# Optimization experiments

Measured on AMD Instinct MI355X. Metric: run time of the kernel, lower is better.

## Reference

```python
import jax, jax.numpy as jnp
import numpy as np

B, T, D, H = 64, 2048, 256, 256

def setup_inputs() -> dict:
    key = jax.random.key(0)
    k_x, k_z, k_r, k_h = jax.random.split(key, 4)
    gate_in = D + H
    # lecun_normal: std = 1/sqrt(fan_in)
    s = 1.0 / np.sqrt(gate_in)
    return {
        "x": jax.random.normal(k_x, (B, T, D), dtype=jnp.float32),
        "W_z": jax.random.normal(k_z, (gate_in, H), dtype=jnp.float32) * s,
        "b_z": jnp.zeros((H,), dtype=jnp.float32),
        "W_r": jax.random.normal(k_r, (gate_in, H), dtype=jnp.float32) * s,
        "b_r": jnp.zeros((H,), dtype=jnp.float32),
        "W_h": jax.random.normal(k_h, (gate_in, H), dtype=jnp.float32) * s,
        "b_h": jnp.zeros((H,), dtype=jnp.float32),
    }

def reference(x, W_z, b_z, W_r, b_r, W_h, b_h):
    Bx, Tx, Dx = x.shape
    Hx = W_z.shape[1]

    def scan_fn(h_prev, x_t):
        xh = jnp.concatenate([x_t, h_prev], axis=-1)        # [B, D+H]
        z = jax.nn.sigmoid(xh @ W_z + b_z)                   # [B, H]
        r = jax.nn.sigmoid(xh @ W_r + b_r)                   # [B, H]
        xrh = jnp.concatenate([x_t, r * h_prev], axis=-1)   # [B, D+H]
        h_hat = jnp.tanh(xrh @ W_h + b_h)                    # [B, H]
        h_new = (1 - z) * h_prev + z * h_hat
        return h_new, h_new

    h0 = jnp.zeros((Bx, Hx), dtype=x.dtype)
    x_t = jnp.transpose(x, (1, 0, 2))                        # [T, B, D]
    _, all_h = jax.lax.scan(scan_fn, h0, x_t)                # [T, B, H]
    return jnp.transpose(all_h, (1, 0, 2))                   # [B, T, H]
```

## Files before the change

kernel.cpp:

```cpp
#include <hip/hip_runtime.h>

typedef _Float16 half2_t __attribute__((ext_vector_type(2)));

#define NB 64
#define NT 2048
#define ND 256
#define NH 256
#define NTHR 256
#define CHUNK 32
#define NCHUNK (NT / CHUNK)

#define XT_STRIDE 132
#define LDS_DW (32 * XT_STRIDE + 16)
#define VQ_BYTE 256

__device__ __forceinline__ float sigmoid_f(float x) { return 1.f / (1.f + __expf(-x)); }
__device__ __forceinline__ float tanh_f(float x)    { return 1.f - 2.f / (1.f + __expf(2.f * x)); }
__device__ __forceinline__ half2_t mkh2(float a, float b) {
    half2_t r; r.x = (_Float16)a; r.y = (_Float16)b; return r;
}
__device__ __forceinline__ half2_t u2h2(unsigned u) { return __builtin_bit_cast(half2_t, u); }
__device__ __forceinline__ float h2get(unsigned u, int idx) {
    half2_t h = u2h2(u);
    return idx ? (float)h.y : (float)h.x;
}
__device__ __forceinline__ int dot4i8(int a, int b, int c) {
#if __has_builtin(__builtin_amdgcn_sdot4)
    return __builtin_amdgcn_sdot4(a, b, c, false);
#else
    int d;
    asm("v_dot4_i32_i8 %0, %1, %2, %3" : "=v"(d) : "v"(a), "v"(b), "v"(c));
    return d;
#endif
}
#define BAR_LDS() asm volatile("s_waitcnt lgkmcnt(0)\n\ts_barrier" ::: "memory")

extern "C" __global__ void __launch_bounds__(NTHR)
gru_fused(const float* __restrict__ x,
          const float* __restrict__ Wz, const float* __restrict__ bz,
          const float* __restrict__ Wr, const float* __restrict__ br,
          const float* __restrict__ Wh, const float* __restrict__ bh,
          float* __restrict__ out,
          unsigned* prodflag, unsigned* consflag,
          unsigned long long* preZR, unsigned* preH, int ring)
{
    __shared__ __align__(16) unsigned smem[LDS_DW];
    const int tid = threadIdx.x;
    const int bid = blockIdx.x;
    const int rmask = ring - 1;

    if (bid >= NB) {
        const int pb = bid - NB;
        const int g  = pb >> 6;
        const int b  = pb & 63;
        const float* W    = (g == 0) ? Wz : (g == 1) ? Wr : Wh;
        const float* bias = (g == 0) ? bz : (g == 1) ? br : bh;
        const int kh = tid & 1;
        const int c2 = tid >> 1;
        const int c0 = c2 * 2, c1 = c0 + 1;

        half2_t wa[64], wb[64];
        #pragma unroll
        for (int j = 0; j < 64; ++j) {
            const int k = kh * 128 + 2 * j;
            wa[j] = mkh2(W[k * NH + c0], W[(k + 1) * NH + c0]);
            wb[j] = mkh2(W[k * NH + c1], W[(k + 1) * NH + c1]);
        }
        const float bv0 = bias[c0], bv1 = bias[c1];

        for (int ch = 0; ch < NCHUNK; ++ch) {
            const int lead = ch * CHUNK + CHUNK - ring;
            if (lead > 0) {
                if (tid == 0) {
                    unsigned it = 0;
                    while ((int)__hip_atomic_load(&consflag[b], __ATOMIC_RELAXED,
                                                  __HIP_MEMORY_SCOPE_AGENT) < lead) {
                        __builtin_amdgcn_s_sleep(8);
                        if (++it > (1u << 20)) break;
                    }
                }
                __syncthreads();
            }
            const int t0 = ch * CHUNK;
            {
                const float4* xs = reinterpret_cast<const float4*>(
                    x + (size_t)b * NT * ND + (size_t)t0 * ND);
                #pragma unroll
                for (int rep = 0; rep < 8; ++rep) {
                    const int f = rep * NTHR + tid;
                    const float4 v = xs[f];
                    const int tt = f >> 6;
                    const int u2 = f & 63;
                    uint2 pk;
                    pk.x = __builtin_bit_cast(unsigned, mkh2(v.x, v.y));
                    pk.y = __builtin_bit_cast(unsigned, mkh2(v.z, v.w));
                    *reinterpret_cast<uint2*>(&smem[tt * XT_STRIDE + u2 * 2]) = pk;
                }
            }
            __syncthreads();
            #pragma unroll 1
            for (int t = 0; t < CHUNK; ++t) {
                const uint4* xr4 = reinterpret_cast<const uint4*>(
                    &smem[t * XT_STRIDE + kh * 64]);
                float a00 = 0.f, a01 = 0.f, a10 = 0.f, a11 = 0.f;
                #pragma unroll
                for (int i = 0; i < 16; ++i) {
                    const uint4 xv = xr4[i];
                    a00 = __builtin_amdgcn_fdot2(u2h2(xv.x), wa[i*4+0], a00, false);
                    a01 = __builtin_amdgcn_fdot2(u2h2(xv.y), wa[i*4+1], a01, false);
                    a00 = __builtin_amdgcn_fdot2(u2h2(xv.z), wa[i*4+2], a00, false);
                    a01 = __builtin_amdgcn_fdot2(u2h2(xv.w), wa[i*4+3], a01, false);
                    a10 = __builtin_amdgcn_fdot2(u2h2(xv.x), wb[i*4+0], a10, false);
                    a11 = __builtin_amdgcn_fdot2(u2h2(xv.y), wb[i*4+1], a11, false);
                    a10 = __builtin_amdgcn_fdot2(u2h2(xv.z), wb[i*4+2], a10, false);
                    a11 = __builtin_amdgcn_fdot2(u2h2(xv.w), wb[i*4+3], a11, false);
                }
                float a0 = a00 + a01, a1 = a10 + a11;
                a0 += __shfl_xor(a0, 1, 64);
                a1 += __shfl_xor(a1, 1, 64);
                a0 += bv0; a1 += bv1;
                if (kh == 0) {
                    const unsigned pk = __builtin_bit_cast(unsigned, mkh2(a0, a1));
                    const size_t slot = (size_t)b * ring + ((t0 + t) & rmask);
                    if (g == 2) {
                        __hip_atomic_store(&preH[slot * 128 + c2], pk,
                                           __ATOMIC_RELAXED, __HIP_MEMORY_SCOPE_AGENT);
                    } else {
                        unsigned* zr32 = reinterpret_cast<unsigned*>(&preZR[slot * 128 + c2]);
                        __hip_atomic_store(&zr32[g], pk,
                                           __ATOMIC_RELAXED, __HIP_MEMORY_SCOPE_AGENT);
                    }
                }
            }
            asm volatile("s_waitcnt vmcnt(0)" ::: "memory");
            __syncthreads();
            if (tid == 0)
                __hip_atomic_store(&prodflag[b * 3 + g], (unsigned)(ch + 1),
                                   __ATOMIC_RELAXED, __HIP_MEMORY_SCOPE_AGENT);
            __syncthreads();
        }
        return;
    }

    const int b    = bid;
    const int c    = tid;
    const int lane = tid & 63;
    const int sub  = c & 1;

    float mxz = 1e-8f, mxr = 1e-8f, mxh = 1e-8f;
    #pragma unroll 4
    for (int j = 0; j < 256; ++j) {
        mxz = fmaxf(mxz, fabsf(Wz[(ND + j) * NH + c]));
        mxr = fmaxf(mxr, fabsf(Wr[(ND + j) * NH + c]));
        mxh = fmaxf(mxh, fabsf(Wh[(ND + j) * NH + c]));
    }
    const float qsz = 127.0f / mxz, qsr = 127.0f / mxr, qsh = 127.0f / mxh;
    const float deqz = mxz / (127.0f * 127.0f);
    const float deqr = mxr / (127.0f * 127.0f);
    const float deqh = mxh / (127.0f * 127.0f);

    uint4 wz4[16], wr4[16], wh4[16];
    #pragma unroll
    for (int i = 0; i < 16; ++i) {
        unsigned dz[4], dr[4], dh[4];
        #pragma unroll
        for (int d = 0; d < 4; ++d) {
            unsigned az = 0, ar = 0, ah = 0;
            #pragma unroll
            for (int j = 0; j < 4; ++j) {
                const int k = ND + (i * 4 + d) * 4 + j;
                const int qz = __float2int_rn(Wz[k * NH + c] * qsz);
                const int qr = __float2int_rn(Wr[k * NH + c] * qsr);
                const int qh = __float2int_rn(Wh[k * NH + c] * qsh);
                az |= ((unsigned)(qz & 255)) << (8 * j);
                ar |= ((unsigned)(qr & 255)) << (8 * j);
                ah |= ((unsigned)(qh & 255)) << (8 * j);
            }
            dz[d] = az; dr[d] = ar; dh[d] = ah;
        }
        wz4[i] = make_uint4(dz[0], dz[1], dz[2], dz[3]);
        wr4[i] = make_uint4(dr[0], dr[1], dr[2], dr[3]);
        wh4[i] = make_uint4(dh[0], dh[1], dh[2], dh[3]);
    }

    if (tid < 128) smem[tid] = 0u;
    float hreg = 0.f;

    if (tid < 3) {
        unsigned it = 0;
        while (__hip_atomic_load(&prodflag[b * 3 + tid], __ATOMIC_RELAXED,
                                 __HIP_MEMORY_SCOPE_AGENT) < 1u) {
            __builtin_amdgcn_s_sleep(8);
            if (++it > (1u << 20)) break;
        }
    }
    __syncthreads();

    const unsigned long long* zrb = preZR + (size_t)b * ring * 128 + (c >> 1);
    const unsigned*           hhb = preH  + (size_t)b * ring * 128 + (c >> 1);
    float* outb = out + (size_t)b * NT * NH + c;
    const uint4* hq4 = reinterpret_cast<const uint4*>(smem);
    const uint4* vq4 = reinterpret_cast<const uint4*>(
                           reinterpret_cast<const char*>(smem) + VQ_BYTE);
    char* hqb = reinterpret_cast<char*>(smem);

    unsigned long long zr_c = __hip_atomic_load(zrb, __ATOMIC_RELAXED, __HIP_MEMORY_SCOPE_AGENT);
    unsigned           hh_c = __hip_atomic_load(hhb, __ATOMIC_RELAXED, __HIP_MEMORY_SCOPE_AGENT);

    auto step = [&](int t) {
        const uint4 hvec = hq4[lane & 15];
        int az0 = 0, az1 = 0, az2 = 0, az3 = 0;
        int ar0 = 0, ar1 = 0, ar2 = 0, ar3 = 0;
        #pragma unroll
        for (int i = 0; i < 16; ++i) {
            const int sx = __builtin_amdgcn_readlane((int)hvec.x, i);
            const int sy = __builtin_amdgcn_readlane((int)hvec.y, i);
            const int sz = __builtin_amdgcn_readlane((int)hvec.z, i);
            const int sw = __builtin_amdgcn_readlane((int)hvec.w, i);
            az0 = dot4i8(sx, (int)wz4[i].x, az0);
            az1 = dot4i8(sy, (int)wz4[i].y, az1);
            az2 = dot4i8(sz, (int)wz4[i].z, az2);
            az3 = dot4i8(sw, (int)wz4[i].w, az3);
            ar0 = dot4i8(sx, (int)wr4[i].x, ar0);
            ar1 = dot4i8(sy, (int)wr4[i].y, ar1);
            ar2 = dot4i8(sz, (int)wr4[i].z, ar2);
            ar3 = dot4i8(sw, (int)wr4[i].w, ar3);
        }
        const float azf = (float)((az0 + az1) + (az2 + az3)) * deqz
                        + h2get((unsigned)(zr_c & 0xffffffffu), sub);
        const float arf = (float)((ar0 + ar1) + (ar2 + ar3)) * deqr;
        const float r = sigmoid_f(arf + h2get((unsigned)(zr_c >> 32), sub));
        const float v = r * hreg;
        hqb[VQ_BYTE + c] = (char)__float2int_rn(v * 127.0f);
        BAR_LDS();

        const float z = sigmoid_f(azf);
        const uint4 vvec = vq4[lane & 15];
        int ah0 = 0, ah1 = 0, ah2 = 0, ah3 = 0;
        #pragma unroll
        for (int i = 0; i < 16; ++i) {
            const int sx = __builtin_amdgcn_readlane((int)vvec.x, i);
            const int sy = __builtin_amdgcn_readlane((int)vvec.y, i);
            const int sz = __builtin_amdgcn_readlane((int)vvec.z, i);
            const int sw = __builtin_amdgcn_readlane((int)vvec.w, i);
            ah0 = dot4i8(sx, (int)wh4[i].x, ah0);
            ah1 = dot4i8(sy, (int)wh4[i].y, ah1);
            ah2 = dot4i8(sz, (int)wh4[i].z, ah2);
            ah3 = dot4i8(sw, (int)wh4[i].w, ah3);
        }
        const float ahf = (float)((ah0 + ah1) + (ah2 + ah3)) * deqh;
        const float hhat = tanh_f(ahf + h2get(hh_c, sub));
        const float hn = hreg + z * (hhat - hreg);
        hreg = hn;
        hqb[c] = (char)__float2int_rn(hn * 127.0f);
        outb[(size_t)t * NH] = hn;
        BAR_LDS();
    };
    auto prefetch = [&](int t, unsigned long long& zr_n, unsigned& hh_n) {
        const int so = (t & rmask) * 128;
        zr_n = __hip_atomic_load(zrb + so, __ATOMIC_RELAXED, __HIP_MEMORY_SCOPE_AGENT);
        hh_n = __hip_atomic_load(hhb + so, __ATOMIC_RELAXED, __HIP_MEMORY_SCOPE_AGENT);
    };

    #pragma unroll 1
    for (int t = 0; t < NT; t += 4) {
        if (t && !(t & (CHUNK - 1))) {
            if (tid == 0)
                __hip_atomic_store(&consflag[b], (unsigned)t,
                                   __ATOMIC_RELAXED, __HIP_MEMORY_SCOPE_AGENT);
            const unsigned need = (unsigned)((t >> 5) + 1);
            if (tid < 3) {
                unsigned it = 0;
                while (__hip_atomic_load(&prodflag[b * 3 + tid], __ATOMIC_RELAXED,
                                         __HIP_MEMORY_SCOPE_AGENT) < need) {
                    __builtin_amdgcn_s_sleep(8);
                    if (++it > (1u << 20)) break;
                }
            }
            __syncthreads();
            prefetch(t, zr_c, hh_c);
        }
        unsigned long long zr_n; unsigned hh_n;
        prefetch(t + 1, zr_n, hh_n);
        step(t);
        zr_c = zr_n; hh_c = hh_n;
        prefetch(t + 2, zr_n, hh_n);
        step(t + 1);
        zr_c = zr_n; hh_c = hh_n;
        prefetch(t + 3, zr_n, hh_n);
        step(t + 2);
        zr_c = zr_n; hh_c = hh_n;
        const int t4 = t + 4;
        const bool pf4 = (t4 < NT) && ((t4 & (CHUNK - 1)) != 0);
        if (pf4) prefetch(t4, zr_n, hh_n);
        step(t + 3);
        if (pf4) { zr_c = zr_n; hh_c = hh_n; }
    }
}

extern "C" void kernel_launch(void* const* d_in, const int* in_sizes, int n_in,
                              void* d_out, int out_size, void* d_ws, size_t ws_size,
                              hipStream_t stream) {
    const float* x  = (const float*)d_in[0];
    const float* Wz = (const float*)d_in[1];
    const float* bz = (const float*)d_in[2];
    const float* Wr = (const float*)d_in[3];
    const float* br = (const float*)d_in[4];
    const float* Wh = (const float*)d_in[5];
    const float* bh = (const float*)d_in[6];
    float* outp = (float*)d_out;

    const size_t base = 4096;
    int ring = 32;
    for (int r = 64; r >= 32; r >>= 1) {
        const size_t need = base + (size_t)NB * r * 128 * 12;
        if (need <= ws_size) { ring = r; break; }
    }
    char* w = (char*)d_ws;
    unsigned* prodflag = (unsigned*)w;
    unsigned* consflag = (unsigned*)(w + 1024);
    unsigned long long* preZR = (unsigned long long*)(w + base);
    unsigned* preH = (unsigned*)(w + base + (size_t)NB * ring * 128 * 8);

    hipMemsetAsync(w, 0, 4096, stream);
    gru_fused<<<256, NTHR, 0, stream>>>(x, Wz, bz, Wr, br, Wh, bh, outp,
                                        prodflag, consflag, preZR, preH, ring);
}
```

Before: 1.900 ms.

## Split recurrent GRU gates across 512 threads with LDS partial-sum exchange

After: 2.972 ms. +56.5%, slower.

```diff
diff --git a/kernel.cpp b/kernel.cpp
--- a/kernel.cpp
+++ b/kernel.cpp
@@ -6,13 +6,16 @@
 #define NT 2048
 #define ND 256
 #define NH 256
-#define NTHR 256
+#define NTHR 512
 #define CHUNK 32
 #define NCHUNK (NT / CHUNK)
 
 #define XT_STRIDE 132
 #define LDS_DW (32 * XT_STRIDE + 16)
 #define VQ_BYTE 256
+#define AZX_OFF 128
+#define AH0_OFF 384
+#define AH1_OFF 640
 
 __device__ __forceinline__ float sigmoid_f(float x) { return 1.f / (1.f + __expf(-x)); }
 __device__ __forceinline__ float tanh_f(float x)    { return 1.f - 2.f / (1.f + __expf(2.f * x)); }
@@ -55,18 +58,15 @@
         const int b  = pb & 63;
         const float* W    = (g == 0) ? Wz : (g == 1) ? Wr : Wh;
         const float* bias = (g == 0) ? bz : (g == 1) ? br : bh;
+        const int c  = tid >> 1;
         const int kh = tid & 1;
-        const int c2 = tid >> 1;
-        const int c0 = c2 * 2, c1 = c0 + 1;
-
-        half2_t wa[64], wb[64];
-        #pragma unroll
-        for (int j = 0; j < 64; ++j) {
-            const int k = kh * 128 + 2 * j;
-            wa[j] = mkh2(W[k * NH + c0], W[(k + 1) * NH + c0]);
-            wb[j] = mkh2(W[k * NH + c1], W[(k + 1) * NH + c1]);
-        }
-        const float bv0 = bias[c0], bv1 = bias[c1];
+
+        half2_t w2[64];
+        #pragma unroll
+        for (int j = 0; j < 64; ++j)
+            w2[j] = mkh2(W[(kh * 128 + 2 * j) * NH + c],
+                         W[(kh * 128 + 2 * j + 1) * NH + c]);
+        const float bv = bias[c];
 
         for (int ch = 0; ch < NCHUNK; ++ch) {
             const int lead = ch * CHUNK + CHUNK - ring;
@@ -84,9 +84,9 @@
             const int t0 = ch * CHUNK;
             {
                 const float4* xs = reinterpret_cast<const float4*>(
-                    x + (size_t)b * NT * ND + (size_t)t0 * ND);
+                    x + ((size_t)b * NT + t0) * ND);
                 #pragma unroll
-                for (int rep = 0; rep < 8; ++rep) {
+                for (int rep = 0; rep < 4; ++rep) {
                     const int f = rep * NTHR + tid;
                     const float4 v = xs[f];
                     const int tt = f >> 6;
@@ -102,31 +102,27 @@
             for (int t = 0; t < CHUNK; ++t) {
                 const uint4* xr4 = reinterpret_cast<const uint4*>(
                     &smem[t * XT_STRIDE + kh * 64]);
-                float a00 = 0.f, a01 = 0.f, a10 = 0.f, a11 = 0.f;
+                float a0 = 0.f, a1 = 0.f, a2 = 0.f, a3 = 0.f;
                 #pragma unroll
                 for (int i = 0; i < 16; ++i) {
                     const uint4 xv = xr4[i];
-                    a00 = __builtin_amdgcn_fdot2(u2h2(xv.x), wa[i*4+0], a00, false);
-                    a01 = __builtin_amdgcn_fdot2(u2h2(xv.y), wa[i*4+1], a01, false);
-                    a00 = __builtin_amdgcn_fdot2(u2h2(xv.z), wa[i*4+2], a00, false);
-                    a01 = __builtin_amdgcn_fdot2(u2h2(xv.w), wa[i*4+3], a01, false);
-                    a10 = __builtin_amdgcn_fdot2(u2h2(xv.x), wb[i*4+0], a10, false);
-                    a11 = __builtin_amdgcn_fdot2(u2h2(xv.y), wb[i*4+1], a11, false);
-                    a10 = __builtin_amdgcn_fdot2(u2h2(xv.z), wb[i*4+2], a10, false);
-                    a11 = __builtin_amdgcn_fdot2(u2h2(xv.w), wb[i*4+3], a11, false);
-                }
-                float a0 = a00 + a01, a1 = a10 + a11;
-                a0 += __shfl_xor(a0, 1, 64);
-                a1 += __shfl_xor(a1, 1, 64);
-                a0 += bv0; a1 += bv1;
-                if (kh == 0) {
-                    const unsigned pk = __builtin_bit_cast(unsigned, mkh2(a0, a1));
+                    a0 = __builtin_amdgcn_fdot2(u2h2(xv.x), w2[i*4+0], a0, false);
+                    a1 = __builtin_amdgcn_fdot2(u2h2(xv.y), w2[i*4+1], a1, false);
+                    a2 = __builtin_amdgcn_fdot2(u2h2(xv.z), w2[i*4+2], a2, false);
+                    a3 = __builtin_amdgcn_fdot2(u2h2(xv.w), w2[i*4+3], a3, false);
+                }
+                float a = (a0 + a1) + (a2 + a3);
+                a += __shfl_xor(a, 1, 64);
+                a += bv;
+                const float an = __shfl_xor(a, 2, 64);
+                if (!(tid & 3)) {
+                    const unsigned pk = __builtin_bit_cast(unsigned, mkh2(a, an));
                     const size_t slot = (size_t)b * ring + ((t0 + t) & rmask);
                     if (g == 2) {
-                        __hip_atomic_store(&preH[slot * 128 + c2], pk,
+                        __hip_atomic_store(&preH[slot * 128 + (c >> 1)], pk,
                                            __ATOMIC_RELAXED, __HIP_MEMORY_SCOPE_AGENT);
                     } else {
-                        unsigned* zr32 = reinterpret_cast<unsigned*>(&preZR[slot * 128 + c2]);
+                        unsigned* zr32 = reinterpret_cast<unsigned*>(&preZR[slot * 128 + (c >> 1)]);
                         __hip_atomic_store(&zr32[g], pk,
                                            __ATOMIC_RELAXED, __HIP_MEMORY_SCOPE_AGENT);
                     }
@@ -143,44 +139,57 @@
     }
 
     const int b    = bid;
-    const int c    = tid;
+    const int p    = tid >> 8;
+    const int c    = tid & 255;
     const int lane = tid & 63;
     const int sub  = c & 1;
 
-    float mxz = 1e-8f, mxr = 1e-8f, mxh = 1e-8f;
+    const float* Wm = p ? Wr : Wz;
+    float mxm = 1e-8f, mxh = 1e-8f;
     #pragma unroll 4
-    for (int j = 0; j < 256; ++j) {
-        mxz = fmaxf(mxz, fabsf(Wz[(ND + j) * NH + c]));
-        mxr = fmaxf(mxr, fabsf(Wr[(ND + j) * NH + c]));
-        mxh = fmaxf(mxh, fabsf(Wh[(ND + j) * NH + c]));
-    }
-    const float qsz = 127.0f / mxz, qsr = 127.0f / mxr, qsh = 127.0f / mxh;
-    const float deqz = mxz / (127.0f * 127.0f);
-    const float deqr = mxr / (127.0f * 127.0f);
+    for (int j = 0; j < 256; ++j) mxm = fmaxf(mxm, fabsf(Wm[(ND + j) * NH + c]));
+    {
+        const int kb = ND + p * 128;
+        #pragma unroll 4
+        for (int j = 0; j < 128; ++j) mxh = fmaxf(mxh, fabsf(Wh[(kb + j) * NH + c]));
+    }
+    const float qsm = 127.0f / mxm, qsh = 127.0f / mxh;
+    const float deqm = mxm / (127.0f * 127.0f);
     const float deqh = mxh / (127.0f * 127.0f);
 
-    uint4 wz4[16], wr4[16], wh4[16];
+    uint4 wm4[16];
     #pragma unroll
     for (int i = 0; i < 16; ++i) {
-        unsigned dz[4], dr[4], dh[4];
+        unsigned d4[4];
         #pragma unroll
         for (int d = 0; d < 4; ++d) {
-            unsigned az = 0, ar = 0, ah = 0;
+            unsigned a = 0;
             #pragma unroll
             for (int j = 0; j < 4; ++j) {
                 const int k = ND + (i * 4 + d) * 4 + j;
-                const int qz = __float2int_rn(Wz[k * NH + c] * qsz);
-                const int qr = __float2int_rn(Wr[k * NH + c] * qsr);
-                const int qh = __float2int_rn(Wh[k * NH + c] * qsh);
-                az |= ((unsigned)(qz & 255)) << (8 * j);
-                ar |= ((unsigned)(qr & 255)) << (8 * j);
-                ah |= ((unsigned)(qh & 255)) << (8 * j);
-            }
-            dz[d] = az; dr[d] = ar; dh[d] = ah;
-        }
-        wz4[i] = make_uint4(dz[0], dz[1], dz[2], dz[3]);
-        wr4[i] = make_uint4(dr[0], dr[1], dr[2], dr[3]);
-        wh4[i] = make_uint4(dh[0], dh[1], dh[2], dh[3]);
+                const int q = __float2int_rn(Wm[k * NH + c] * qsm);
+                a |= ((unsigned)(q & 255)) << (8 * j);
+            }
+            d4[d] = a;
+        }
+        wm4[i] = make_uint4(d4[0], d4[1], d4[2], d4[3]);
+    }
+    uint4 wh4[8];
+    #pragma unroll
+    for (int i = 0; i < 8; ++i) {
+        unsigned d4[4];
+        #pragma unroll
+        for (int d = 0; d < 4; ++d) {
+            unsigned a = 0;
+            #pragma unroll
+            for (int j = 0; j < 4; ++j) {
+                const int k = ND + p * 128 + (i * 4 + d) * 4 + j;
+                const int q = __float2int_rn(Wh[k * NH + c] * qsh);
+                a |= ((unsigned)(q & 255)) << (8 * j);
+            }
+            d4[d] = a;
+        }
+        wh4[i] = make_uint4(d4[0], d4[1], d4[2], d4[3]);
     }
 
     if (tid < 128) smem[tid] = 0u;
@@ -203,57 +212,64 @@
     const uint4* vq4 = reinterpret_cast<const uint4*>(
                            reinterpret_cast<const char*>(smem) + VQ_BYTE);
     char* hqb = reinterpret_cast<char*>(smem);
+    float* azx  = reinterpret_cast<float*>(smem + AZX_OFF);
+    float* ah0x = reinterpret_cast<float*>(smem + AH0_OFF);
+    float* ah1x = reinterpret_cast<float*>(smem + AH1_OFF);
 
     unsigned long long zr_c = __hip_atomic_load(zrb, __ATOMIC_RELAXED, __HIP_MEMORY_SCOPE_AGENT);
     unsigned           hh_c = __hip_atomic_load(hhb, __ATOMIC_RELAXED, __HIP_MEMORY_SCOPE_AGENT);
 
     auto step = [&](int t) {
         const uint4 hvec = hq4[lane & 15];
-        int az0 = 0, az1 = 0, az2 = 0, az3 = 0;
-        int ar0 = 0, ar1 = 0, ar2 = 0, ar3 = 0;
+        int a0 = 0, a1 = 0, a2 = 0, a3 = 0;
         #pragma unroll
         for (int i = 0; i < 16; ++i) {
             const int sx = __builtin_amdgcn_readlane((int)hvec.x, i);
             const int sy = __builtin_amdgcn_readlane((int)hvec.y, i);
             const int sz = __builtin_amdgcn_readlane((int)hvec.z, i);
             const int sw = __builtin_amdgcn_readlane((int)hvec.w, i);
-            az0 = dot4i8(sx, (int)wz4[i].x, az0);
-            az1 = dot4i8(sy, (int)wz4[i].y, az1);
-            az2 = dot4i8(sz, (int)wz4[i].z, az2);
-            az3 = dot4i8(sw, (int)wz4[i].w, az3);
-            ar0 = dot4i8(sx, (int)wr4[i].x, ar0);
-            ar1 = dot4i8(sy, (int)wr4[i].y, ar1);
-            ar2 = dot4i8(sz, (int)wr4[i].z, ar2);
-            ar3 = dot4i8(sw, (int)wr4[i].w, ar3);
-        }
-        const float azf = (float)((az0 + az1) + (az2 + az3)) * deqz
-                        + h2get((unsigned)(zr_c & 0xffffffffu), sub);
-        const float arf = (float)((ar0 + ar1) + (ar2 + ar3)) * deqr;
-        const float r = sigmoid_f(arf + h2get((unsigned)(zr_c >> 32), sub));
-        const float v = r * hreg;
-        hqb[VQ_BYTE + c] = (char)__float2int_rn(v * 127.0f);
+            a0 = dot4i8(sx, (int)wm4[i].x, a0);
+            a1 = dot4i8(sy, (int)wm4[i].y, a1);
+            a2 = dot4i8(sz, (int)wm4[i].z, a2);
+            a3 = dot4i8(sw, (int)wm4[i].w, a3);
+        }
+        const float pre_m = p ? h2get((unsigned)(zr_c >> 32), sub)
+                              : h2get((unsigned)(zr_c & 0xffffffffu), sub);
+        const float amf = (float)((a0 + a1) + (a2 + a3)) * deqm + pre_m;
+        if (p) {
+            const float r = sigmoid_f(amf);
+            const float v = r * hreg;
+            hqb[VQ_BYTE + c] = (char)__float2int_rn(v * 127.0f);
+        }
         BAR_LDS();
 
-        const float z = sigmoid_f(azf);
         const uint4 vvec = vq4[lane & 15];
-        int ah0 = 0, ah1 = 0, ah2 = 0, ah3 = 0;
-        #pragma unroll
-        for (int i = 0; i < 16; ++i) {
-            const int sx = __builtin_amdgcn_readlane((int)vvec.x, i);
-            const int sy = __builtin_amdgcn_readlane((int)vvec.y, i);
-            const int sz = __builtin_amdgcn_readlane((int)vvec.z, i);
-            const int sw = __builtin_amdgcn_readlane((int)vvec.w, i);
-            ah0 = dot4i8(sx, (int)wh4[i].x, ah0);
-            ah1 = dot4i8(sy, (int)wh4[i].y, ah1);
-            ah2 = dot4i8(sz, (int)wh4[i].z, ah2);
-            ah3 = dot4i8(sw, (int)wh4[i].w, ah3);
-        }
-        const float ahf = (float)((ah0 + ah1) + (ah2 + ah3)) * deqh;
+        int h0 = 0, h1 = 0, h2 = 0, h3 = 0;
+        #pragma unroll
+        for (int i = 0; i < 8; ++i) {
+            const int li = p * 8 + i;
+            const int sx = __builtin_amdgcn_readlane((int)vvec.x, li);
+            const int sy = __builtin_amdgcn_readlane((int)vvec.y, li);
+            const int sz = __builtin_amdgcn_readlane((int)vvec.z, li);
+            const int sw = __builtin_amdgcn_readlane((int)vvec.w, li);
+            h0 = dot4i8(sx, (int)wh4[i].x, h0);
+            h1 = dot4i8(sy, (int)wh4[i].y, h1);
+            h2 = dot4i8(sz, (int)wh4[i].z, h2);
+            h3 = dot4i8(sw, (int)wh4[i].w, h3);
+        }
+        const float ahp = (float)((h0 + h1) + (h2 + h3)) * deqh;
+        if (p) { ah1x[c] = ahp; }
+        else   { ah0x[c] = ahp; azx[c] = amf; }
+        BAR_LDS();
+
+        const float ahf = p ? (ah0x[c] + ahp) : (ahp + ah1x[c]);
+        const float zf  = p ? azx[c] : amf;
+        const float z = sigmoid_f(zf);
         const float hhat = tanh_f(ahf + h2get(hh_c, sub));
         const float hn = hreg + z * (hhat - hreg);
         hreg = hn;
-        hqb[c] = (char)__float2int_rn(hn * 127.0f);
-        outb[(size_t)t * NH] = hn;
+        if (p) hqb[c] = (char)__float2int_rn(hn * 127.0f);
+        else   outb[(size_t)t * NH] = hn;
         BAR_LDS();
     };
     auto prefetch = [&](int t, unsigned long long& zr_n, unsigned& hh_n) {
```
